# Performance work log

Measured on AMD Instinct MI355X. Metric: run time of the kernel, lower is better.

## Reference

```python
import jax, jax.numpy as jnp
import numpy as np

H_SIZE = 2048
N_HEADS = 16
N_KV = 4
HEAD_DIM = 128
EPS = 1e-6
ROPE_THETA = 10000.0


def _rms_norm(x, w):
    # per-head RMSNorm over last dim (head_dim)
    var = jnp.mean(jnp.square(x), axis=-1, keepdims=True)
    return x * jax.lax.rsqrt(var + EPS) * w


def _rope(x, positions):
    # neox-style rotary over full head_dim. x: [B,S,H,D], positions: [B,S]
    d = x.shape[-1]
    inv_freq = 1.0 / (ROPE_THETA ** (jnp.arange(0, d, 2, dtype=jnp.float32) / d))
    ang = positions.astype(jnp.float32)[..., None] * inv_freq  # [B,S,D/2]
    cos = jnp.cos(ang)[:, :, None, :]
    sin = jnp.sin(ang)[:, :, None, :]
    x1, x2 = x[..., : d // 2], x[..., d // 2 :]
    return jnp.concatenate([x1 * cos - x2 * sin, x2 * cos + x1 * sin], axis=-1)


def setup_inputs() -> dict:
    key = jax.random.key(0)
    k1, k2, k3 = jax.random.split(key, 3)
    B, S = 2, 2048
    positions = jnp.broadcast_to(jnp.arange(S, dtype=jnp.int32), (B, S))
    hidden_states = jax.random.normal(k1, (B, S, H_SIZE), dtype=jnp.float32)
    w_qkv = jax.random.normal(k2, (H_SIZE, (N_HEADS + 2 * N_KV) * HEAD_DIM), dtype=jnp.float32) * 0.02
    w_o = jax.random.normal(k3, (N_HEADS * HEAD_DIM, H_SIZE), dtype=jnp.float32) * 0.02
    q_norm_w = jnp.ones((HEAD_DIM,), dtype=jnp.float32)
    k_norm_w = jnp.ones((HEAD_DIM,), dtype=jnp.float32)
    return {"positions": positions, "hidden_states": hidden_states, "w_qkv": w_qkv,
            "w_o": w_o, "q_norm_w": q_norm_w, "k_norm_w": k_norm_w}


def reference(positions, hidden_states, w_qkv, w_o, q_norm_w, k_norm_w):
    B, S, _ = hidden_states.shape
    q_size = N_HEADS * HEAD_DIM
    kv_size = N_KV * HEAD_DIM
    qkv = hidden_states @ w_qkv  # [B,S,q+2kv]
    q = qkv[..., :q_size].reshape(B, S, N_HEADS, HEAD_DIM)
    k = qkv[..., q_size : q_size + kv_size].reshape(B, S, N_KV, HEAD_DIM)
    v = qkv[..., q_size + kv_size :].reshape(B, S, N_KV, HEAD_DIM)
    q = _rms_norm(q, q_norm_w)
    k = _rms_norm(k, k_norm_w)
    q = _rope(q, positions)
    k = _rope(k, positions)
    # GQA: repeat kv heads
    rep = N_HEADS // N_KV
    k = jnp.repeat(k, rep, axis=2)
    v = jnp.repeat(v, rep, axis=2)
    scale = HEAD_DIM ** -0.5
    scores = jnp.einsum("bqhd,bkhd->bhqk", q, k) * scale
    causal = jnp.tril(jnp.ones((S, S), dtype=bool))
    scores = jnp.where(causal, scores, jnp.finfo(scores.dtype).min)
    probs = jax.nn.softmax(scores, axis=-1)
    attn = jnp.einsum("bhqk,bkhd->bqhd", probs, v).reshape(B, S, N_HEADS * HEAD_DIM)
    return attn @ w_o
```

## Files before the change

kernel.cpp:

```cpp
#include <hip/hip_runtime.h>
#include <math.h>

#define TOKS 4096
#define HS   2048
#define QKV_N 3072
#define S_LEN 2048
#define NH   16
#define NKV  4
#define DH   128

typedef __attribute__((ext_vector_type(8))) short short8;
typedef __attribute__((ext_vector_type(4))) float f32x4;

static __device__ __forceinline__ unsigned short f2bf(float f) {
  unsigned u = __builtin_bit_cast(unsigned, f);
  u += 0x7fffu + ((u >> 16) & 1u);
  return (unsigned short)(u >> 16);
}

__global__ __launch_bounds__(256)
void cvt_bf16(const float* __restrict__ in, unsigned short* __restrict__ out) {
  const size_t i = ((size_t)blockIdx.x * 256 + threadIdx.x) * 8;
  float4 a = *(const float4*)(in + i);
  float4 b = *(const float4*)(in + i + 4);
  short8 r;
  r[0] = f2bf(a.x); r[1] = f2bf(a.y); r[2] = f2bf(a.z); r[3] = f2bf(a.w);
  r[4] = f2bf(b.x); r[5] = f2bf(b.y); r[6] = f2bf(b.z); r[7] = f2bf(b.w);
  *(short8*)(out + i) = r;
}

__global__ __launch_bounds__(256)
void transpose_cvt(const float* __restrict__ in, unsigned short* __restrict__ out,
                   int R, int C, int ldin,
                   long in_z_hi, long in_z_lo, int z_mod, long out_z) {
  __shared__ float tile[32][33];
  const int z = blockIdx.z;
  in  += (size_t)(z / z_mod) * in_z_hi + (size_t)(z % z_mod) * in_z_lo;
  out += (size_t)z * out_z;
  const int r0 = blockIdx.x * 32, c0 = blockIdx.y * 32;
  const int tx = threadIdx.x & 31, ty = threadIdx.x >> 5;
  #pragma unroll
  for (int i = 0; i < 4; ++i)
    tile[ty + i * 8][tx] = in[(size_t)(r0 + ty + i * 8) * ldin + c0 + tx];
  __syncthreads();
  #pragma unroll
  for (int i = 0; i < 4; ++i)
    out[(size_t)(c0 + ty + i * 8) * R + r0 + tx] = f2bf(tile[tx][ty + i * 8]);
}

__global__ __launch_bounds__(64)
void norm_rope_cvt(const float* __restrict__ qkv, const int* __restrict__ positions,
                   const float* __restrict__ qw, const float* __restrict__ kw,
                   unsigned short* __restrict__ Qb, unsigned short* __restrict__ Kb) {
  const int tok  = blockIdx.x;
  const int slot = blockIdx.y;
  const int lane = threadIdx.x;
  const int b = tok >> 11, s = tok & 2047;

  const float* x; const float* wgt; unsigned short* outp; float scale;
  if (slot < NH) {
    x = qkv + (size_t)tok * QKV_N + slot * DH;  wgt = qw;
    outp = Qb + (((size_t)b * NH + slot) * S_LEN + s) * DH;
    scale = 0.08838834764831845f;
  } else {
    const int kh = slot - NH;
    x = qkv + (size_t)tok * QKV_N + NH * DH + kh * DH;  wgt = kw;
    outp = Kb + (((size_t)b * NKV + kh) * S_LEN + s) * DH;
    scale = 1.0f;
  }

  float x1 = x[lane], x2 = x[lane + 64];
  float ss = x1 * x1 + x2 * x2;
  #pragma unroll
  for (int o = 32; o > 0; o >>= 1) ss += __shfl_xor(ss, o, 64);
  const float rs = 1.0f / sqrtf(ss * (1.0f / 128.0f) + 1e-6f);
  const float n1 = x1 * rs * wgt[lane];
  const float n2 = x2 * rs * wgt[lane + 64];

  const float pos = (float)positions[tok];
  const float inv_freq = exp2f(-(float)lane * (13.287712379549449f / 64.0f));
  float sn, cs;
  sincosf(pos * inv_freq, &sn, &cs);

  outp[lane]      = f2bf((n1 * cs - n2 * sn) * scale);
  outp[lane + 64] = f2bf((n2 * cs + n1 * sn) * scale);
}

__global__ __launch_bounds__(256)
void gemm_bf16(const unsigned short* __restrict__ A, const unsigned short* __restrict__ Bt,
               float* __restrict__ C, int M, int N, int K) {
  __shared__ unsigned short As[128 * 32];
  __shared__ unsigned short Bs[128 * 32];
  const int t = threadIdx.x, w = t >> 6, l = t & 63;
  const int lm = l & 15, lr = l >> 4;
  const int bn = blockIdx.x * 128, bm = blockIdx.y * 128;
  const int wr = w >> 1, wc = w & 1;

  f32x4 acc[4][4];
  #pragma unroll
  for (int i = 0; i < 4; ++i)
    #pragma unroll
    for (int j = 0; j < 4; ++j) acc[i][j] = {0.f, 0.f, 0.f, 0.f};

  const int srow = l >> 2;
  const int scol = (l & 3) * 8;

  for (int k0 = 0; k0 < K; k0 += 32) {
    #pragma unroll
    for (int c = 0; c < 2; ++c) {
      const int rowA = (w + c * 4) * 16;
      const unsigned short* ga = A + (size_t)(bm + rowA + srow) * K + k0 + scol;
      const unsigned short* gb = Bt + (size_t)(bn + rowA + srow) * K + k0 + scol;
      __builtin_amdgcn_global_load_lds(
          (const __attribute__((address_space(1))) void*)ga,
          (__attribute__((address_space(3))) void*)(As + rowA * 32), 16, 0, 0);
      __builtin_amdgcn_global_load_lds(
          (const __attribute__((address_space(1))) void*)gb,
          (__attribute__((address_space(3))) void*)(Bs + rowA * 32), 16, 0, 0);
    }
    __syncthreads();

    short8 af[4], bf[4];
    #pragma unroll
    for (int mi = 0; mi < 4; ++mi)
      af[mi] = *(const short8*)(As + (wr * 64 + mi * 16 + lm) * 32 + lr * 8);
    #pragma unroll
    for (int ni = 0; ni < 4; ++ni)
      bf[ni] = *(const short8*)(Bs + (wc * 64 + ni * 16 + lm) * 32 + lr * 8);
    #pragma unroll
    for (int mi = 0; mi < 4; ++mi)
      #pragma unroll
      for (int ni = 0; ni < 4; ++ni)
        acc[mi][ni] = __builtin_amdgcn_mfma_f32_16x16x32_bf16(af[mi], bf[ni], acc[mi][ni], 0, 0, 0);
    __syncthreads();
  }

  #pragma unroll
  for (int mi = 0; mi < 4; ++mi)
    #pragma unroll
    for (int ni = 0; ni < 4; ++ni)
      #pragma unroll
      for (int j = 0; j < 4; ++j)
        C[(size_t)(bm + wr * 64 + mi * 16 + lr * 4 + j) * N + bn + wc * 64 + ni * 16 + lm] =
            acc[mi][ni][j];
}

#define M_INIT 12.0f
#define P_CAP  2981.0f

__global__ __launch_bounds__(256, 3)
void attn_mfma(const unsigned short* __restrict__ Qb, const unsigned short* __restrict__ Kb,
               const unsigned short* __restrict__ Vt, unsigned short* __restrict__ att) {
  __shared__ unsigned short Ks_[2][64 * 128];
  __shared__ unsigned short Vs_[2][128 * 64];
  __shared__ unsigned short Pl[4][32 * 64];

  const int x  = blockIdx.x;
  const int b  = blockIdx.z;
  const int qb = b ? x : 15 - x;
  const int h  = blockIdx.y;
  const int kvh = h >> 2;
  const int t = threadIdx.x, w = t >> 6, l = t & 63;
  const int lm = l & 15, lr = l >> 4;
  const int row0 = qb * 128 + w * 32;

  const unsigned short* qbase = Qb + ((size_t)(b * NH + h)) * S_LEN * DH;
  const unsigned short* kbase = Kb + ((size_t)(b * NKV + kvh)) * S_LEN * DH;
  const unsigned short* vtbase = Vt + ((size_t)(b * NKV + kvh)) * DH * S_LEN;

  short8 qf[2][4];
  #pragma unroll
  for (int m = 0; m < 2; ++m)
    #pragma unroll
    for (int kc = 0; kc < 4; ++kc)
      qf[m][kc] = *(const short8*)(qbase + (size_t)(row0 + m * 16 + lm) * DH + kc * 32 + lr * 8);

  short8 ones;
  #pragma unroll
  for (int i = 0; i < 8; ++i) ones[i] = (short)0x3F80;

  f32x4 o[2][8];
  #pragma unroll
  for (int m = 0; m < 2; ++m)
    #pragma unroll
    for (int ng = 0; ng < 8; ++ng) o[m][ng] = {0.f, 0.f, 0.f, 0.f};
  f32x4 lacc[2];
  lacc[0] = {0.f, 0.f, 0.f, 0.f}; lacc[1] = {0.f, 0.f, 0.f, 0.f};
  float m_run[2][4];
  #pragma unroll
  for (int m = 0; m < 2; ++m)
    #pragma unroll
    for (int j = 0; j < 4; ++j) m_run[m][j] = M_INIT;

  auto stage = [&](int bufi, int kb0) {
    #pragma unroll
    for (int i = 0; i < 4; ++i) {
      const int rk = w * 16 + i * 4 + (l >> 4);
      const unsigned short* gk =
          kbase + (size_t)(kb0 + rk) * DH + (((l & 15) ^ (rk & 7)) * 8);
      __builtin_amdgcn_global_load_lds(
          (const __attribute__((address_space(1))) void*)gk,
          (__attribute__((address_space(3))) void*)(&Ks_[bufi][(w * 16 + i * 4) * 128]),
          16, 0, 0);
      const int rv = w * 32 + i * 8 + (l >> 3);
      const unsigned short* gv =
          vtbase + (size_t)rv * S_LEN + kb0 + (((l & 7) ^ (rv & 7)) * 8);
      __builtin_amdgcn_global_load_lds(
          (const __attribute__((address_space(1))) void*)gv,
          (__attribute__((address_space(3))) void*)(&Vs_[bufi][(w * 32 + i * 8) * 64]),
          16, 0, 0);
    }
  };

  const int nkt = qb * 2 + 2;
  stage(0, 0);
  __syncthreads();

  for (int kt = 0; kt < nkt; ++kt) {
    const int kb0 = kt * 64;
    if (kt + 1 < nkt) stage((kt + 1) & 1, kb0 + 64);

    if (kb0 <= row0 + 31) {
      const unsigned short* Kc = Ks_[kt & 1];
      const unsigned short* Vc = Vs_[kt & 1];
      const int rsw = (lm & 7) << 3;

      f32x4 s[2][4];
      #pragma unroll
      for (int m = 0; m < 2; ++m)
        #pragma unroll
        for (int n2 = 0; n2 < 4; ++n2) s[m][n2] = {0.f, 0.f, 0.f, 0.f};
      __builtin_amdgcn_s_setprio(1);
      #pragma unroll
      for (int n2 = 0; n2 < 4; ++n2) {
        short8 kf[4];
        #pragma unroll
        for (int kc = 0; kc < 4; ++kc)
          kf[kc] = *(const short8*)(Kc + (n2 * 16 + lm) * 128 + ((kc * 32 + lr * 8) ^ rsw));
        #pragma unroll
        for (int m = 0; m < 2; ++m)
          #pragma unroll
          for (int kc = 0; kc < 4; ++kc)
            s[m][n2] = __builtin_amdgcn_mfma_f32_16x16x32_bf16(qf[m][kc], kf[kc], s[m][n2], 0, 0, 0);
      }
      __builtin_amdgcn_s_setprio(0);

      if (kb0 + 63 > row0) {
        #pragma unroll
        for (int m = 0; m < 2; ++m) {
          const int qi = row0 + m * 16 + lr * 4;
          #pragma unroll
          for (int n2 = 0; n2 < 4; ++n2) {
            const int kvi = kb0 + n2 * 16 + lm;
            #pragma unroll
            for (int j = 0; j < 4; ++j)
              if (kvi > qi + j) s[m][n2][j] = -1e30f;
          }
        }
      }

      float pm = 0.f;
      #pragma unroll
      for (int m = 0; m < 2; ++m)
        #pragma unroll
        for (int n2 = 0; n2 < 4; ++n2)
          #pragma unroll
          for (int j = 0; j < 4; ++j) {
            const float p = __expf(s[m][n2][j] - m_run[m][j]);
            s[m][n2][j] = p;
            pm = fmaxf(pm, p);
          }

      if (!__all(pm <= P_CAP)) {
        #pragma unroll
        for (int m = 0; m < 2; ++m)
          #pragma unroll
          for (int j = 0; j < 4; ++j) {
            float v = fmaxf(fmaxf(s[m][0][j], s[m][1][j]), fmaxf(s[m][2][j], s[m][3][j]));
            v = fmaxf(v, __shfl_xor(v, 1, 64));
            v = fmaxf(v, __shfl_xor(v, 2, 64));
            v = fmaxf(v, __shfl_xor(v, 4, 64));
            v = fmaxf(v, __shfl_xor(v, 8, 64));
            if (v > P_CAP) {
              const float al = 1.0f / v;
              m_run[m][j] += __logf(v);
              lacc[m][j] *= al;
              #pragma unroll
              for (int n2 = 0; n2 < 4; ++n2) s[m][n2][j] *= al;
              #pragma unroll
              for (int ng = 0; ng < 8; ++ng) o[m][ng][j] *= al;
            }
          }
      }

      #pragma unroll
      for (int m = 0; m < 2; ++m)
        #pragma unroll
        for (int j = 0; j < 4; ++j) {
          const int prow = m * 16 + lr * 4 + j;
          unsigned short* Pw = &Pl[w][prow * 64];
          const int sw = (prow & 7) << 3;
          Pw[lm ^ sw]        = f2bf(s[m][0][j]);
          Pw[(16 + lm) ^ sw] = f2bf(s[m][1][j]);
          Pw[(32 + lm) ^ sw] = f2bf(s[m][2][j]);
          Pw[(48 + lm) ^ sw] = f2bf(s[m][3][j]);
        }
      __asm__ volatile("s_waitcnt lgkmcnt(0)" ::: "memory");

      short8 pf[2][2];
      #pragma unroll
      for (int m = 0; m < 2; ++m)
        #pragma unroll
        for (int k2 = 0; k2 < 2; ++k2)
          pf[m][k2] = *(const short8*)(&Pl[w][(m * 16 + lm) * 64 + ((k2 * 32 + lr * 8) ^ rsw)]);
      __builtin_amdgcn_s_setprio(1);
      #pragma unroll
      for (int m = 0; m < 2; ++m)
        #pragma unroll
        for (int k2 = 0; k2 < 2; ++k2)
          lacc[m] = __builtin_amdgcn_mfma_f32_16x16x32_bf16(pf[m][k2], ones, lacc[m], 0, 0, 0);
      #pragma unroll
      for (int ng = 0; ng < 8; ++ng) {
        const short8 vf0 = *(const short8*)(Vc + (ng * 16 + lm) * 64 + ((lr * 8) ^ rsw));
        const short8 vf1 = *(const short8*)(Vc + (ng * 16 + lm) * 64 + ((32 + lr * 8) ^ rsw));
        o[0][ng] = __builtin_amdgcn_mfma_f32_16x16x32_bf16(pf[0][0], vf0, o[0][ng], 0, 0, 0);
        o[1][ng] = __builtin_amdgcn_mfma_f32_16x16x32_bf16(pf[1][0], vf0, o[1][ng], 0, 0, 0);
        o[0][ng] = __builtin_amdgcn_mfma_f32_16x16x32_bf16(pf[0][1], vf1, o[0][ng], 0, 0, 0);
        o[1][ng] = __builtin_amdgcn_mfma_f32_16x16x32_bf16(pf[1][1], vf1, o[1][ng], 0, 0, 0);
      }
      __builtin_amdgcn_s_setprio(0);
    }
    __syncthreads();
  }

  #pragma unroll
  for (int m = 0; m < 2; ++m)
    #pragma unroll
    for (int j = 0; j < 4; ++j) {
      const float linv = 1.0f / lacc[m][j];
      unsigned short* ar =
          att + ((size_t)(b * S_LEN) + row0 + m * 16 + lr * 4 + j) * (NH * DH) + h * DH + lm;
      #pragma unroll
      for (int ng = 0; ng < 8; ++ng) ar[ng * 16] = f2bf(o[m][ng][j] * linv);
    }
}

extern "C" void kernel_launch(void* const* d_in, const int* in_sizes, int n_in,
                              void* d_out, int out_size, void* d_ws, size_t ws_size,
                              hipStream_t stream) {
  const int*   positions = (const int*)  d_in[0];
  const float* hidden    = (const float*)d_in[1];
  const float* w_qkv     = (const float*)d_in[2];
  const float* w_o       = (const float*)d_in[3];
  const float* q_norm_w  = (const float*)d_in[4];
  const float* k_norm_w  = (const float*)d_in[5];
  float* out = (float*)d_out;

  char* ws = (char*)d_ws;
  float*          qkv   = (float*)ws;
  unsigned short* att   = (unsigned short*)ws;
  char* region = ws + (size_t)TOKS * QKV_N * 4;
  unsigned short* hb    = (unsigned short*)region;
  unsigned short* Qb    = (unsigned short*)region;
  unsigned short* wqkvt = (unsigned short*)(region + 16777216);
  unsigned short* Kb    = (unsigned short*)(region + 16777216);
  unsigned short* Vt    = (unsigned short*)(region + 20971520);
  unsigned short* wot   = (unsigned short*)(region + 25165824);

  cvt_bf16<<<(TOKS * HS) / (256 * 8), 256, 0, stream>>>(hidden, hb);
  transpose_cvt<<<dim3(HS / 32, QKV_N / 32, 1), 256, 0, stream>>>(
      w_qkv, wqkvt, HS, QKV_N, QKV_N, 0, 0, 1, 0);
  gemm_bf16<<<dim3(QKV_N / 128, TOKS / 128), 256, 0, stream>>>(
      hb, wqkvt, qkv, TOKS, QKV_N, HS);
  norm_rope_cvt<<<dim3(TOKS, NH + NKV), 64, 0, stream>>>(
      qkv, positions, q_norm_w, k_norm_w, Qb, Kb);
  transpose_cvt<<<dim3(S_LEN / 32, DH / 32, 2 * NKV), 256, 0, stream>>>(
      qkv + (NH + NKV) * DH, Vt, S_LEN, DH, QKV_N,
      (long)S_LEN * QKV_N, DH, NKV, (long)DH * S_LEN);
  transpose_cvt<<<dim3(HS / 32, HS / 32, 1), 256, 0, stream>>>(
      w_o, wot, HS, HS, HS, 0, 0, 1, 0);
  attn_mfma<<<dim3(16, NH, 2), 256, 0, stream>>>(Qb, Kb, Vt, att);
  gemm_bf16<<<dim3(HS / 128, TOKS / 128), 256, 0, stream>>>(
      att, wot, out, TOKS, HS, HS);
}
```

Measured before the change: 294.8 us.

## Replace GEMM with 256x256 double-buffered, swizzled, software-pipelined MFMA kernel

Replaces the simple 128x128, K=32 single-buffered GEMM with a 256x256 tile, K=64, 512-thread kernel. Global-to-LDS loads are double-buffered and interleaved with the MFMA phases, using XOR-swizzled LDS rows to avoid bank conflicts and s_setprio around the MFMA bursts. The goal is to hide memory latency and raise data reuse in both projection GEMMs. In exchange it uses much more LDS and more registers, and the larger tiles give fewer blocks: 192 and 128 in the two grids.

```diff
diff --git a/kernel.cpp b/kernel.cpp
--- a/kernel.cpp
+++ b/kernel.cpp
@@ -86,62 +86,117 @@
   outp[lane + 64] = f2bf((n2 * cs + n1 * sn) * scale);
 }
 
-__global__ __launch_bounds__(256)
-void gemm_bf16(const unsigned short* __restrict__ A, const unsigned short* __restrict__ Bt,
-               float* __restrict__ C, int M, int N, int K) {
-  __shared__ unsigned short As[128 * 32];
-  __shared__ unsigned short Bs[128 * 32];
+__global__ __launch_bounds__(512, 2)
+void gemm256(const unsigned short* __restrict__ A, const unsigned short* __restrict__ Bt,
+             float* __restrict__ C, int M, int N, int K) {
+  __shared__ __align__(16) unsigned short LA[2][256 * 64];
+  __shared__ __align__(16) unsigned short LB[2][256 * 64];
+
   const int t = threadIdx.x, w = t >> 6, l = t & 63;
   const int lm = l & 15, lr = l >> 4;
-  const int bn = blockIdx.x * 128, bm = blockIdx.y * 128;
-  const int wr = w >> 1, wc = w & 1;
-
-  f32x4 acc[4][4];
-  #pragma unroll
-  for (int i = 0; i < 4; ++i)
-    #pragma unroll
-    for (int j = 0; j < 4; ++j) acc[i][j] = {0.f, 0.f, 0.f, 0.f};
-
-  const int srow = l >> 2;
-  const int scol = (l & 3) * 8;
-
-  for (int k0 = 0; k0 < K; k0 += 32) {
-    #pragma unroll
-    for (int c = 0; c < 2; ++c) {
-      const int rowA = (w + c * 4) * 16;
-      const unsigned short* ga = A + (size_t)(bm + rowA + srow) * K + k0 + scol;
-      const unsigned short* gb = Bt + (size_t)(bn + rowA + srow) * K + k0 + scol;
+  const int wr = w >> 2, wc = w & 3;
+  const int bn = blockIdx.x * 256, bm = blockIdx.y * 256;
+  const int nkt = K >> 6;
+
+  f32x4 acc[8][4];
+  #pragma unroll
+  for (int mi = 0; mi < 8; ++mi)
+    #pragma unroll
+    for (int ni = 0; ni < 4; ++ni) acc[mi][ni] = {0.f, 0.f, 0.f, 0.f};
+
+  auto stage = [&](const unsigned short* G, int gbase, unsigned short* Lb,
+                   int half, int kt) {
+    if (kt >= nkt) return;
+    const int k0 = kt << 6;
+    #pragma unroll
+    for (int r = 0; r < 2; ++r) {
+      const int row  = half * 128 + r * 64 + (t >> 3);
+      const int slot = (t & 7) ^ (row & 7);
+      const unsigned short* src = G + (size_t)(gbase + row) * K + k0 + slot * 8;
       __builtin_amdgcn_global_load_lds(
-          (const __attribute__((address_space(1))) void*)ga,
-          (__attribute__((address_space(3))) void*)(As + rowA * 32), 16, 0, 0);
-      __builtin_amdgcn_global_load_lds(
-          (const __attribute__((address_space(1))) void*)gb,
-          (__attribute__((address_space(3))) void*)(Bs + rowA * 32), 16, 0, 0);
+          (const __attribute__((address_space(1))) void*)src,
+          (__attribute__((address_space(3))) void*)(Lb + (half * 128 + r * 64 + w * 8) * 64),
+          16, 0, 0);
     }
-    __syncthreads();
-
-    short8 af[4], bf[4];
-    #pragma unroll
-    for (int mi = 0; mi < 4; ++mi)
-      af[mi] = *(const short8*)(As + (wr * 64 + mi * 16 + lm) * 32 + lr * 8);
+  };
+
+  stage(Bt, bn, &LB[0][0], 0, 0); stage(Bt, bn, &LB[0][0], 1, 0);
+  stage(A,  bm, &LA[0][0], 0, 0); stage(A,  bm, &LA[0][0], 1, 0);
+  stage(Bt, bn, &LB[1][0], 0, 1); stage(Bt, bn, &LB[1][0], 1, 1);
+  asm volatile("s_waitcnt vmcnt(4)" ::: "memory");
+  __builtin_amdgcn_s_barrier();
+
+  const int niter = nkt >> 1;
+  for (int i = 0; i < niter; ++i) {
+    const int t0 = i * 2;
+    short8 bfr[4][2];
+    #pragma unroll
+    for (int p = 0; p < 8; ++p) {
+      const int buf = p >> 2, q = p & 3;
+      const unsigned short* La = &LA[buf][0];
+      const unsigned short* Lb = &LB[buf][0];
+
+      if (q == 0) {
+        #pragma unroll
+        for (int ni = 0; ni < 4; ++ni)
+          #pragma unroll
+          for (int ks = 0; ks < 2; ++ks) {
+            const int row = wc * 64 + ni * 16 + lm;
+            bfr[ni][ks] = *(const short8*)(Lb + row * 64 +
+                                           ((ks * 32 + lr * 8) ^ ((row & 7) << 3)));
+          }
+      }
+      short8 af[2][2];
+      #pragma unroll
+      for (int mi2 = 0; mi2 < 2; ++mi2)
+        #pragma unroll
+        for (int ks = 0; ks < 2; ++ks) {
+          const int row = wr * 128 + (q * 2 + mi2) * 16 + lm;
+          af[mi2][ks] = *(const short8*)(La + row * 64 +
+                                         ((ks * 32 + lr * 8) ^ ((row & 7) << 3)));
+        }
+
+      switch (p) {
+        case 0: stage(A,  bm, &LA[1][0], 0, t0 + 1); break;
+        case 1: stage(A,  bm, &LA[1][0], 1, t0 + 1); break;
+        case 2: stage(Bt, bn, &LB[0][0], 0, t0 + 2); break;
+        case 3: stage(Bt, bn, &LB[0][0], 1, t0 + 2); break;
+        case 4: stage(A,  bm, &LA[0][0], 0, t0 + 2); break;
+        case 5: stage(A,  bm, &LA[0][0], 1, t0 + 2); break;
+        case 6: stage(Bt, bn, &LB[1][0], 0, t0 + 3); break;
+        case 7: stage(Bt, bn, &LB[1][0], 1, t0 + 3); break;
+      }
+
+      __builtin_amdgcn_s_barrier();
+      asm volatile("s_waitcnt lgkmcnt(0)" ::: "memory");
+      __builtin_amdgcn_sched_barrier(0);
+
+      __builtin_amdgcn_s_setprio(1);
+      #pragma unroll
+      for (int mi2 = 0; mi2 < 2; ++mi2)
+        #pragma unroll
+        for (int ni = 0; ni < 4; ++ni)
+          #pragma unroll
+          for (int ks = 0; ks < 2; ++ks)
+            acc[q * 2 + mi2][ni] = __builtin_amdgcn_mfma_f32_16x16x32_bf16(
+                af[mi2][ks], bfr[ni][ks], acc[q * 2 + mi2][ni], 0, 0, 0);
+      __builtin_amdgcn_s_setprio(0);
+
+      if (q == 3) {
+        if (i == niter - 1) asm volatile("s_waitcnt vmcnt(0)" ::: "memory");
+        else                asm volatile("s_waitcnt vmcnt(4)" ::: "memory");
+      }
+      __builtin_amdgcn_s_barrier();
+    }
+  }
+
+  #pragma unroll
+  for (int mi = 0; mi < 8; ++mi)
     #pragma unroll
     for (int ni = 0; ni < 4; ++ni)
-      bf[ni] = *(const short8*)(Bs + (wc * 64 + ni * 16 + lm) * 32 + lr * 8);
-    #pragma unroll
-    for (int mi = 0; mi < 4; ++mi)
-      #pragma unroll
-      for (int ni = 0; ni < 4; ++ni)
-        acc[mi][ni] = __builtin_amdgcn_mfma_f32_16x16x32_bf16(af[mi], bf[ni], acc[mi][ni], 0, 0, 0);
-    __syncthreads();
-  }
-
-  #pragma unroll
-  for (int mi = 0; mi < 4; ++mi)
-    #pragma unroll
-    for (int ni = 0; ni < 4; ++ni)
       #pragma unroll
       for (int j = 0; j < 4; ++j)
-        C[(size_t)(bm + wr * 64 + mi * 16 + lr * 4 + j) * N + bn + wc * 64 + ni * 16 + lm] =
+        C[(size_t)(bm + wr * 128 + mi * 16 + lr * 4 + j) * N + bn + wc * 64 + ni * 16 + lm] =
             acc[mi][ni][j];
 }
 
@@ -370,7 +425,7 @@
   cvt_bf16<<<(TOKS * HS) / (256 * 8), 256, 0, stream>>>(hidden, hb);
   transpose_cvt<<<dim3(HS / 32, QKV_N / 32, 1), 256, 0, stream>>>(
       w_qkv, wqkvt, HS, QKV_N, QKV_N, 0, 0, 1, 0);
-  gemm_bf16<<<dim3(QKV_N / 128, TOKS / 128), 256, 0, stream>>>(
+  gemm256<<<dim3(QKV_N / 256, TOKS / 256), 512, 0, stream>>>(
       hb, wqkvt, qkv, TOKS, QKV_N, HS);
   norm_rope_cvt<<<dim3(TOKS, NH + NKV), 64, 0, stream>>>(
       qkv, positions, q_norm_w, k_norm_w, Qb, Kb);
@@ -380,6 +435,6 @@
   transpose_cvt<<<dim3(HS / 32, HS / 32, 1), 256, 0, stream>>>(
       w_o, wot, HS, HS, HS, 0, 0, 1, 0);
   attn_mfma<<<dim3(16, NH, 2), 256, 0, stream>>>(Qb, Kb, Vt, att);
-  gemm_bf16<<<dim3(HS / 128, TOKS / 128), 256, 0, stream>>>(
+  gemm256<<<dim3(HS / 256, TOKS / 256), 512, 0, stream>>>(
       att, wot, out, TOKS, HS, HS);
 }
```

After: 284.4 us. -3.5%, faster.
